# Performance work log

Measured on AMD Instinct MI355X. Metric: run time of the kernel, lower is better.

The kernel has to match this reference:

```python
import jax, jax.numpy as jnp
import numpy as np

FEATURE_DIM = 128
BATCH = 2
SEQ = 512  # single domain region (0, SEQ) per batch element


def setup_inputs() -> dict:
    key = jax.random.key(0)
    ks = jax.random.split(key, 8)
    D = FEATURE_DIM
    s = lambda fan_in: 1.0 / np.sqrt(fan_in)
    return {
        "domain_features": jax.random.normal(ks[0], (BATCH, SEQ, D), jnp.float32),
        "evolutionary_features": jax.random.normal(ks[1], (BATCH, SEQ, D), jnp.float32),
        # pattern_detector params (jax convention: W is [in, out])
        "W1": jax.random.uniform(ks[2], (2 * D, D), jnp.float32, -s(2 * D), s(2 * D)),
        "b1": jax.random.uniform(ks[3], (D,), jnp.float32, -s(2 * D), s(2 * D)),
        "W2": jax.random.uniform(ks[4], (D, D // 2), jnp.float32, -s(D), s(D)),
        "b2": jax.random.uniform(ks[5], (D // 2,), jnp.float32, -s(D), s(D)),
        "W3": jax.random.uniform(ks[6], (D // 2, 1), jnp.float32, -s(D // 2), s(D // 2)),
        "b3": jax.random.uniform(ks[7], (1,), jnp.float32, -s(D // 2), s(D // 2)),
    }


def reference(domain_features, evolutionary_features, W1, b1, W2, b2, W3, b3):
    D = domain_features.shape[-1]
    # per-position combined feature: g_i = domain_feat[i] * evo_feat[i]
    g = domain_features * evolutionary_features  # [B, N, D]
    # Linear(2D -> D) on cat(g_i, g_j) splits into two halves of W1
    a = jnp.einsum("bnd,de->bne", g, W1[:D])  # contribution of position i
    c = jnp.einsum("bnd,de->bne", g, W1[D:])  # contribution of position j
    h = jax.nn.relu(a[:, :, None, :] + c[:, None, :, :] + b1)       # [B, N, N, D]
    h = jax.nn.relu(jnp.einsum("bijd,de->bije", h, W2) + b2)        # [B, N, N, D//2]
    s = jax.nn.sigmoid(jnp.einsum("bije,e->bij", h, W3[:, 0]) + b3[0])  # [B, N, N]
    # original loop fills only i < j and mirrors; diagonal stays zero
    upper = jnp.triu(s, k=1)
    coevo = upper + jnp.swapaxes(upper, -1, -2)  # symmetric [B, N, N]
    return coevo
```

## Files before the change

kernel.cpp:

```cpp
#include <hip/hip_runtime.h>
#include <hip/hip_bf16.h>

#define D 128
#define Nn 512
#define Bb 2

typedef __bf16 bf16x8_t __attribute__((ext_vector_type(8)));
typedef unsigned short u16x8_t __attribute__((ext_vector_type(8)));
typedef float f32x4_t __attribute__((ext_vector_type(4)));
typedef float f32x8_t __attribute__((ext_vector_type(8)));

__global__ __launch_bounds__(256)
void precompute_ac(const float* __restrict__ dom, const float* __restrict__ evo,
                   const float* __restrict__ W1, const float* __restrict__ b1,
                   const float* __restrict__ W2,
                   __bf16* __restrict__ A16, __bf16* __restrict__ C16,
                   __bf16* __restrict__ W2T) {
    const int t = threadIdx.x;
    const int base = blockIdx.x * 2;
    if (blockIdx.x < 8) {
#pragma unroll
        for (int z = 0; z < 4; ++z) {
            int idx = z * 256 + t;
            int e = blockIdx.x * 8 + (idx >> 7);
            int k = idx & 127;
            W2T[e * 128 + k] = (__bf16)W2[k * 64 + e];
        }
    }
    __shared__ float g2[2][D];
    {
        int r = t >> 7, c = t & 127;
        size_t off = (size_t)(base + r) * D + c;
        g2[r][c] = dom[off] * evo[off];
    }
    __syncthreads();
    const int half = t >> 7;
    const int e = t & 127;
    const float* Wp = W1 + half * D * D;
    float a0 = 0.f, a1 = 0.f;
#pragma unroll 16
    for (int dp = 0; dp < D; ++dp) {
        float w = Wp[dp * D + e];
        a0 = fmaf(g2[0][dp], w, a0);
        a1 = fmaf(g2[1][dp], w, a1);
    }
    if (half == 0) {
        float bb = b1[e];
        A16[(size_t)(base + 0) * D + e] = (__bf16)(a0 + bb);
        A16[(size_t)(base + 1) * D + e] = (__bf16)(a1 + bb);
    } else {
        C16[(size_t)(base + 0) * D + e] = (__bf16)a0;
        C16[(size_t)(base + 1) * D + e] = (__bf16)a1;
    }
}

__device__ __forceinline__ float row16_reduce(float x) {
    int v = __builtin_bit_cast(int, x);
    x += __builtin_bit_cast(float, __builtin_amdgcn_update_dpp(0, v, 0x118, 0xf, 0xf, false));
    v = __builtin_bit_cast(int, x);
    x += __builtin_bit_cast(float, __builtin_amdgcn_update_dpp(0, v, 0x114, 0xf, 0xf, false));
    v = __builtin_bit_cast(int, x);
    x += __builtin_bit_cast(float, __builtin_amdgcn_update_dpp(0, v, 0x112, 0xf, 0xf, false));
    v = __builtin_bit_cast(int, x);
    x += __builtin_bit_cast(float, __builtin_amdgcn_update_dpp(0, v, 0x111, 0xf, 0xf, false));
    return x;
}

__global__ __launch_bounds__(256, 5)
void coevo_main(const __bf16* __restrict__ A16, const __bf16* __restrict__ Cm,
                const __bf16* __restrict__ W2T, const float* __restrict__ b2,
                const float* __restrict__ W3, const float* __restrict__ b3,
                float* __restrict__ out) {
    const int tid  = threadIdx.x;
    const int wave = tid >> 6;
    const int lane = tid & 63;
    const int m = lane & 15;
    const int q = lane >> 4;

    int u = blockIdx.x;
    const int b = (u >= 576) ? 1 : 0;
    u -= b * 576;
    int chunk = 0;
#pragma unroll
    for (int cc = 1; cc < 8; ++cc) if (u >= 8 * cc * (cc + 1)) chunk = cc;
    const int g = u - 8 * chunk * (chunk + 1);
    const int i = g * 4 + wave;
    const int i0 = g * 4;

    __shared__ __bf16 w2s[64 * 128];
    __shared__ float  tile[4][64];

    const u16x8_t* Ag8 = (const u16x8_t*)(A16 + ((size_t)(b * Nn + i)) * D);
    u16x8_t ab16[4];
#pragma unroll
    for (int kk = 0; kk < 4; ++kk) ab16[kk] = Ag8[kk * 4 + q];

    {
        f32x4_t* w2v = (f32x4_t*)w2s;
        const f32x4_t* W2Tg = (const f32x4_t*)W2T;
#pragma unroll
        for (int it = 0; it < 4; ++it) {
            int f = it * 256 + tid;
            int r = f >> 4, gi = f & 15;
            w2v[r * 16 + (gi ^ (r & 15))] = W2Tg[f];
        }
    }

    f32x8_t abv[4];
#pragma unroll
    for (int kk = 0; kk < 4; ++kk) {
#pragma unroll
        for (int z = 0; z < 8; ++z)
            abv[kk][z] = __builtin_bit_cast(float, (unsigned)ab16[kk][z] << 16);
    }

    float b2v[4], w3v[4];
#pragma unroll
    for (int et = 0; et < 4; ++et) {
        b2v[et] = b2[et * 16 + m];
        w3v[et] = W3[et * 16 + m];
    }
    const float b3s = b3[0];

    __syncthreads();

    const u16x8_t*  Cg8 = (const u16x8_t*)(Cm + ((size_t)b * Nn + (size_t)chunk * 64) * D);
    const bf16x8_t* w2r = (const bf16x8_t*)w2s;

#pragma unroll
    for (int jt = 0; jt < 4; ++jt) {
        if (chunk * 64 + jt * 16 + 15 < i) continue;
        const int r0 = jt * 16 + m;

        bf16x8_t af[4];
#pragma unroll
        for (int kk = 0; kk < 4; ++kk) {
            u16x8_t cr = Cg8[r0 * 16 + kk * 4 + q];
            f32x8_t c8;
#pragma unroll
            for (int z = 0; z < 8; ++z)
                c8[z] = __builtin_bit_cast(float, (unsigned)cr[z] << 16);
            f32x8_t t8 = __builtin_elementwise_max(abv[kk] + c8, (f32x8_t)0.f);
            af[kk] = __builtin_convertvector(t8, bf16x8_t);
        }

        float part[4] = {0.f, 0.f, 0.f, 0.f};
#pragma unroll
        for (int et = 0; et < 4; ++et) {
            bf16x8_t wf[4];
#pragma unroll
            for (int kk = 0; kk < 4; ++kk)
                wf[kk] = w2r[(et * 16 + m) * 16 + ((kk * 4 + q) ^ m)];
            f32x4_t a = {0.f, 0.f, 0.f, 0.f};
#pragma unroll
            for (int kk = 0; kk < 4; ++kk)
                a = __builtin_amdgcn_mfma_f32_16x16x32_bf16(af[kk], wf[kk], a, 0, 0, 0);
#pragma unroll
            for (int r = 0; r < 4; ++r)
                part[r] = fmaf(fmaxf(a[r] + b2v[et], 0.f), w3v[et], part[r]);
        }

        float red[4];
#pragma unroll
        for (int r = 0; r < 4; ++r) red[r] = row16_reduce(part[r]);
        if (m == 15) {
#pragma unroll
            for (int r = 0; r < 4; ++r) {
                int jc = jt * 16 + q * 4 + r;
                tile[wave][jc] = 1.f / (1.f + expf(-(red[r] + b3s)));
            }
        }
    }

    __syncthreads();

    if ((tid & 63) < 16) {
        const int c4 = tid & 15;
        const int j0 = chunk * 64 + c4 * 4;
        float v0 = tile[wave][c4 * 4 + 0];
        float v1 = tile[wave][c4 * 4 + 1];
        float v2 = tile[wave][c4 * 4 + 2];
        float v3 = tile[wave][c4 * 4 + 3];
        float* op = out + ((size_t)b * Nn + i) * Nn + j0;
        if (j0 > i) {
            f32x4_t v; v[0] = v0; v[1] = v1; v[2] = v2; v[3] = v3;
            *(f32x4_t*)op = v;
        } else if (j0 + 3 >= i) {
            if (j0 + 0 > i) op[0] = v0; else if (j0 + 0 == i) op[0] = 0.f;
            if (j0 + 1 > i) op[1] = v1; else if (j0 + 1 == i) op[1] = 0.f;
            if (j0 + 2 > i) op[2] = v2; else if (j0 + 2 == i) op[2] = 0.f;
            if (j0 + 3 > i) op[3] = v3; else if (j0 + 3 == i) op[3] = 0.f;
        }
    }
    if (tid < 64) {
        const int j = chunk * 64 + tid;
        float v0 = tile[0][tid], v1 = tile[1][tid], v2 = tile[2][tid], v3 = tile[3][tid];
        float* op = out + ((size_t)b * Nn + j) * Nn + i0;
        if (j > i0 + 3) {
            f32x4_t v; v[0] = v0; v[1] = v1; v[2] = v2; v[3] = v3;
            *(f32x4_t*)op = v;
        } else {
            if (j > i0 + 0) op[0] = v0;
            if (j > i0 + 1) op[1] = v1;
            if (j > i0 + 2) op[2] = v2;
            if (j > i0 + 3) op[3] = v3;
        }
    }
}

extern "C" void kernel_launch(void* const* d_in, const int* in_sizes, int n_in,
                              void* d_out, int out_size, void* d_ws, size_t ws_size,
                              hipStream_t stream) {
    const float* dom = (const float*)d_in[0];
    const float* evo = (const float*)d_in[1];
    const float* W1  = (const float*)d_in[2];
    const float* b1  = (const float*)d_in[3];
    const float* W2  = (const float*)d_in[4];
    const float* b2  = (const float*)d_in[5];
    const float* W3  = (const float*)d_in[6];
    const float* b3  = (const float*)d_in[7];
    float* out = (float*)d_out;

    __bf16* A16 = (__bf16*)d_ws;
    __bf16* C16 = A16 + (size_t)Bb * Nn * D;
    __bf16* W2T = C16 + (size_t)Bb * Nn * D;

    precompute_ac<<<Bb * Nn / 2, 256, 0, stream>>>(dom, evo, W1, b1, W2, A16, C16, W2T);
    coevo_main<<<Bb * 576, 256, 0, stream>>>(A16, C16, W2T, b2, W3, b3, out);
}
```

Measured before the change: 25.68 us.

## Make coevo_main persistent over three work units with double-buffered tile

New measurement: 32.89 us. +28.1%, slower.

```diff
diff --git a/kernel.cpp b/kernel.cpp
--- a/kernel.cpp
+++ b/kernel.cpp
@@ -6,7 +6,7 @@
 #define Bb 2
 
 typedef __bf16 bf16x8_t __attribute__((ext_vector_type(8)));
-typedef unsigned short u16x8_t __attribute__((ext_vector_type(8)));
+typedef unsigned int u32x4_t __attribute__((ext_vector_type(4)));
 typedef float f32x4_t __attribute__((ext_vector_type(4)));
 typedef float f32x8_t __attribute__((ext_vector_type(8)));
 
@@ -66,7 +66,17 @@
     return x;
 }
 
-__global__ __launch_bounds__(256, 5)
+__device__ __forceinline__ f32x8_t expand_bf16x8(u32x4_t d) {
+    f32x8_t r;
+#pragma unroll
+    for (int z = 0; z < 4; ++z) {
+        r[2 * z]     = __builtin_bit_cast(float, d[z] << 16);
+        r[2 * z + 1] = __builtin_bit_cast(float, d[z] & 0xffff0000u);
+    }
+    return r;
+}
+
+__global__ __launch_bounds__(256, 4)
 void coevo_main(const __bf16* __restrict__ A16, const __bf16* __restrict__ Cm,
                 const __bf16* __restrict__ W2T, const float* __restrict__ b2,
                 const float* __restrict__ W3, const float* __restrict__ b3,
@@ -77,23 +87,8 @@
     const int m = lane & 15;
     const int q = lane >> 4;
 
-    int u = blockIdx.x;
-    const int b = (u >= 576) ? 1 : 0;
-    u -= b * 576;
-    int chunk = 0;
-#pragma unroll
-    for (int cc = 1; cc < 8; ++cc) if (u >= 8 * cc * (cc + 1)) chunk = cc;
-    const int g = u - 8 * chunk * (chunk + 1);
-    const int i = g * 4 + wave;
-    const int i0 = g * 4;
-
     __shared__ __bf16 w2s[64 * 128];
-    __shared__ float  tile[4][64];
-
-    const u16x8_t* Ag8 = (const u16x8_t*)(A16 + ((size_t)(b * Nn + i)) * D);
-    u16x8_t ab16[4];
-#pragma unroll
-    for (int kk = 0; kk < 4; ++kk) ab16[kk] = Ag8[kk * 4 + q];
+    __shared__ float  tile[2][4][64];
 
     {
         f32x4_t* w2v = (f32x4_t*)w2s;
@@ -106,14 +101,6 @@
         }
     }
 
-    f32x8_t abv[4];
-#pragma unroll
-    for (int kk = 0; kk < 4; ++kk) {
-#pragma unroll
-        for (int z = 0; z < 8; ++z)
-            abv[kk][z] = __builtin_bit_cast(float, (unsigned)ab16[kk][z] << 16);
-    }
-
     float b2v[4], w3v[4];
 #pragma unroll
     for (int et = 0; et < 4; ++et) {
@@ -121,89 +108,104 @@
         w3v[et] = W3[et * 16 + m];
     }
     const float b3s = b3[0];
+    const bf16x8_t* w2r = (const bf16x8_t*)w2s;
 
     __syncthreads();
 
-    const u16x8_t*  Cg8 = (const u16x8_t*)(Cm + ((size_t)b * Nn + (size_t)chunk * 64) * D);
-    const bf16x8_t* w2r = (const bf16x8_t*)w2s;
-
-#pragma unroll
-    for (int jt = 0; jt < 4; ++jt) {
-        if (chunk * 64 + jt * 16 + 15 < i) continue;
-        const int r0 = jt * 16 + m;
-
-        bf16x8_t af[4];
-#pragma unroll
-        for (int kk = 0; kk < 4; ++kk) {
-            u16x8_t cr = Cg8[r0 * 16 + kk * 4 + q];
-            f32x8_t c8;
-#pragma unroll
-            for (int z = 0; z < 8; ++z)
-                c8[z] = __builtin_bit_cast(float, (unsigned)cr[z] << 16);
-            f32x8_t t8 = __builtin_elementwise_max(abv[kk] + c8, (f32x8_t)0.f);
-            af[kk] = __builtin_convertvector(t8, bf16x8_t);
-        }
-
-        float part[4] = {0.f, 0.f, 0.f, 0.f};
-#pragma unroll
-        for (int et = 0; et < 4; ++et) {
-            bf16x8_t wf[4];
-#pragma unroll
-            for (int kk = 0; kk < 4; ++kk)
-                wf[kk] = w2r[(et * 16 + m) * 16 + ((kk * 4 + q) ^ m)];
-            f32x4_t a = {0.f, 0.f, 0.f, 0.f};
-#pragma unroll
-            for (int kk = 0; kk < 4; ++kk)
-                a = __builtin_amdgcn_mfma_f32_16x16x32_bf16(af[kk], wf[kk], a, 0, 0, 0);
-#pragma unroll
-            for (int r = 0; r < 4; ++r)
-                part[r] = fmaf(fmaxf(a[r] + b2v[et], 0.f), w3v[et], part[r]);
-        }
-
-        float red[4];
-#pragma unroll
-        for (int r = 0; r < 4; ++r) red[r] = row16_reduce(part[r]);
-        if (m == 15) {
-#pragma unroll
-            for (int r = 0; r < 4; ++r) {
-                int jc = jt * 16 + q * 4 + r;
-                tile[wave][jc] = 1.f / (1.f + expf(-(red[r] + b3s)));
-            }
-        }
-    }
-
-    __syncthreads();
-
-    if ((tid & 63) < 16) {
-        const int c4 = tid & 15;
-        const int j0 = chunk * 64 + c4 * 4;
-        float v0 = tile[wave][c4 * 4 + 0];
-        float v1 = tile[wave][c4 * 4 + 1];
-        float v2 = tile[wave][c4 * 4 + 2];
-        float v3 = tile[wave][c4 * 4 + 3];
-        float* op = out + ((size_t)b * Nn + i) * Nn + j0;
-        if (j0 > i) {
-            f32x4_t v; v[0] = v0; v[1] = v1; v[2] = v2; v[3] = v3;
-            *(f32x4_t*)op = v;
-        } else if (j0 + 3 >= i) {
-            if (j0 + 0 > i) op[0] = v0; else if (j0 + 0 == i) op[0] = 0.f;
-            if (j0 + 1 > i) op[1] = v1; else if (j0 + 1 == i) op[1] = 0.f;
-            if (j0 + 2 > i) op[2] = v2; else if (j0 + 2 == i) op[2] = 0.f;
-            if (j0 + 3 > i) op[3] = v3; else if (j0 + 3 == i) op[3] = 0.f;
-        }
-    }
-    if (tid < 64) {
-        const int j = chunk * 64 + tid;
-        float v0 = tile[0][tid], v1 = tile[1][tid], v2 = tile[2][tid], v3 = tile[3][tid];
-        float* op = out + ((size_t)b * Nn + j) * Nn + i0;
-        if (j > i0 + 3) {
-            f32x4_t v; v[0] = v0; v[1] = v1; v[2] = v2; v[3] = v3;
-            *(f32x4_t*)op = v;
-        } else {
-            if (j > i0 + 0) op[0] = v0;
-            if (j > i0 + 1) op[1] = v1;
-            if (j > i0 + 2) op[2] = v2;
-            if (j > i0 + 3) op[3] = v3;
+    for (int t = 0; t < 3; ++t) {
+        const int p = t & 1;
+        int u = blockIdx.x + 384 * t;
+        const int b = (u >= 576) ? 1 : 0;
+        u -= b * 576;
+        int chunk = 0;
+#pragma unroll
+        for (int cc = 1; cc < 8; ++cc) if (u >= 8 * cc * (cc + 1)) chunk = cc;
+        const int g = u - 8 * chunk * (chunk + 1);
+        const int i = g * 4 + wave;
+        const int i0 = g * 4;
+
+        const u32x4_t* Ag = (const u32x4_t*)(A16 + ((size_t)(b * Nn + i)) * D);
+        f32x8_t abv[4];
+#pragma unroll
+        for (int kk = 0; kk < 4; ++kk) abv[kk] = expand_bf16x8(Ag[kk * 4 + q]);
+
+        const u32x4_t* Cg = (const u32x4_t*)(Cm + ((size_t)b * Nn + (size_t)chunk * 64) * D);
+
+#pragma unroll
+        for (int jt = 0; jt < 4; ++jt) {
+            if (chunk * 64 + jt * 16 + 15 < i) continue;
+            const int r0 = jt * 16 + m;
+
+            bf16x8_t af[4];
+#pragma unroll
+            for (int kk = 0; kk < 4; ++kk) {
+                f32x8_t c8 = expand_bf16x8(Cg[r0 * 16 + kk * 4 + q]);
+                f32x8_t t8 = __builtin_elementwise_max(abv[kk] + c8, (f32x8_t)0.f);
+                af[kk] = __builtin_convertvector(t8, bf16x8_t);
+            }
+
+            float part[4] = {0.f, 0.f, 0.f, 0.f};
+#pragma unroll
+            for (int et = 0; et < 4; ++et) {
+                bf16x8_t wf[4];
+#pragma unroll
+                for (int kk = 0; kk < 4; ++kk)
+                    wf[kk] = w2r[(et * 16 + m) * 16 + ((kk * 4 + q) ^ m)];
+                f32x4_t a = {0.f, 0.f, 0.f, 0.f};
+#pragma unroll
+                for (int kk = 0; kk < 4; ++kk)
+                    a = __builtin_amdgcn_mfma_f32_16x16x32_bf16(af[kk], wf[kk], a, 0, 0, 0);
+#pragma unroll
+                for (int r = 0; r < 4; ++r)
+                    part[r] = fmaf(fmaxf(a[r] + b2v[et], 0.f), w3v[et], part[r]);
+            }
+
+            float red[4];
+#pragma unroll
+            for (int r = 0; r < 4; ++r) red[r] = row16_reduce(part[r]);
+            if (m == 15) {
+#pragma unroll
+                for (int r = 0; r < 4; ++r) {
+                    int jc = jt * 16 + q * 4 + r;
+                    tile[p][wave][jc] = 1.f / (1.f + expf(-(red[r] + b3s)));
+                }
+            }
+        }
+
+        __syncthreads();
+
+        if ((tid & 63) < 16) {
+            const int c4 = tid & 15;
+            const int j0 = chunk * 64 + c4 * 4;
+            float v0 = tile[p][wave][c4 * 4 + 0];
+            float v1 = tile[p][wave][c4 * 4 + 1];
+            float v2 = tile[p][wave][c4 * 4 + 2];
+            float v3 = tile[p][wave][c4 * 4 + 3];
+            float* op = out + ((size_t)b * Nn + i) * Nn + j0;
+            if (j0 > i) {
+                f32x4_t v; v[0] = v0; v[1] = v1; v[2] = v2; v[3] = v3;
+                *(f32x4_t*)op = v;
+            } else if (j0 + 3 >= i) {
+                if (j0 + 0 > i) op[0] = v0; else if (j0 + 0 == i) op[0] = 0.f;
+                if (j0 + 1 > i) op[1] = v1; else if (j0 + 1 == i) op[1] = 0.f;
+                if (j0 + 2 > i) op[2] = v2; else if (j0 + 2 == i) op[2] = 0.f;
+                if (j0 + 3 > i) op[3] = v3; else if (j0 + 3 == i) op[3] = 0.f;
+            }
+        }
+        if (tid < 64) {
+            const int j = chunk * 64 + tid;
+            float v0 = tile[p][0][tid], v1 = tile[p][1][tid];
+            float v2 = tile[p][2][tid], v3 = tile[p][3][tid];
+            float* op = out + ((size_t)b * Nn + j) * Nn + i0;
+            if (j > i0 + 3) {
+                f32x4_t v; v[0] = v0; v[1] = v1; v[2] = v2; v[3] = v3;
+                *(f32x4_t*)op = v;
+            } else {
+                if (j > i0 + 0) op[0] = v0;
+                if (j > i0 + 1) op[1] = v1;
+                if (j > i0 + 2) op[2] = v2;
+                if (j > i0 + 3) op[3] = v3;
+            }
         }
     }
 }
@@ -226,5 +228,5 @@
     __bf16* W2T = C16 + (size_t)Bb * Nn * D;
 
     precompute_ac<<<Bb * Nn / 2, 256, 0, stream>>>(dom, evo, W1, b1, W2, A16, C16, W2T);
-    coevo_main<<<Bb * 576, 256, 0, stream>>>(A16, C16, W2T, b2, W3, b3, out);
-}
+    coevo_main<<<384, 256, 0, stream>>>(A16, C16, W2T, b2, W3, b3, out);
+}
```
